# Performance work log

Hardware: AMD Instinct MI355X
Metric: run time of the kernel (lower is better)

Reference implementation:

```python
import jax, jax.numpy as jnp
import numpy as np

N_NODES = 100000
N_EDGES = 1600000
DIM = 128
N_LAYERS = 3


def setup_inputs() -> dict:
    key = jax.random.key(0)
    ks = jax.random.split(key, 8)
    h0 = jax.random.normal(ks[0], (N_NODES, 117), dtype=jnp.float32)
    src = jax.random.randint(ks[1], (N_EDGES,), 0, N_NODES, dtype=jnp.int32)
    dst = jax.random.randint(ks[2], (N_EDGES,), 0, N_NODES, dtype=jnp.int32)
    s_in = 1.0 / np.sqrt(117.0)
    s_h = 1.0 / np.sqrt(float(DIM))
    W_in = jax.random.uniform(ks[3], (117, DIM), jnp.float32, -s_in, s_in)
    b_in = jax.random.uniform(ks[4], (DIM,), jnp.float32, -s_in, s_in)
    W_self = jax.random.uniform(ks[5], (N_LAYERS, DIM, DIM), jnp.float32, -s_h, s_h)
    W_neigh = jax.random.uniform(ks[6], (N_LAYERS, DIM, DIM), jnp.float32, -s_h, s_h)
    b_sage = jax.random.uniform(ks[7], (N_LAYERS, DIM), jnp.float32, -s_h, s_h)
    return {"h0": h0, "src": src, "dst": dst, "W_in": W_in, "b_in": b_in,
            "W_self": W_self, "W_neigh": W_neigh, "b_sage": b_sage}


def _sage_mean(x, src, dst, Wse, Wne, b):
    # GraphSAGE with mean aggregator: h = x @ W_self + mean_neigh(x) @ W_neigh + b
    neigh_sum = jax.ops.segment_sum(x[src], dst, num_segments=N_NODES)  # [N, D]
    deg = jax.ops.segment_sum(jnp.ones((src.shape[0],), x.dtype), dst,
                              num_segments=N_NODES)  # [N]
    neigh_mean = neigh_sum / jnp.maximum(deg, 1.0)[:, None]
    return x @ Wse + neigh_mean @ Wne + b


def reference(h0, src, dst, W_in, b_in, W_self, W_neigh, b_sage):
    # f_in: Linear(117,128) + Tanh, per node
    h = jnp.tanh(h0 @ W_in + b_in)  # [N, 128]
    # config = [128,'relu'] x 3 -> SAGEConv then relu, three times
    for l in range(N_LAYERS):
        h = _sage_mean(h, src, dst, W_self[l], W_neigh[l], b_sage[l])
        h = jax.nn.relu(h)
    return h
```

## Files before the change

### kernel.cpp

```cpp
#include <hip/hip_runtime.h>
#include <hip/hip_bf16.h>
#include <cstdint>
#include <cstddef>

#define NN 100000
#define NE 1600000
#define DIM 128
#define KIN 117
#define NLAYERS 3
#define NB 98
#define NMAT 7

typedef __attribute__((ext_vector_type(8))) short s16x8;
typedef __attribute__((ext_vector_type(8))) __bf16 bf16x8;
typedef __attribute__((ext_vector_type(4))) float f32x4;

__device__ __forceinline__ unsigned short f2bf(float f) {
  unsigned int u = __float_as_uint(f);
  unsigned int r = (u + 0x7fffu + ((u >> 16) & 1u)) >> 16;
  return (unsigned short)r;
}
__device__ __forceinline__ float bf2f(unsigned short b) {
  return __uint_as_float(((unsigned int)b) << 16);
}


__global__ void k_hist(const int* __restrict__ dst, int* __restrict__ cnt) {
  int i = blockIdx.x * blockDim.x + threadIdx.x;
  if (i < NE) atomicAdd(&cnt[dst[i]], 1);
}

__global__ void k_scanA(const int* __restrict__ cnt, int* __restrict__ part,
                        int* __restrict__ bsum) {
  __shared__ int sh[1024];
  int tid = threadIdx.x;
  int i = blockIdx.x * 1024 + tid;
  int v = (i < NN) ? cnt[i] : 0;
  sh[tid] = v;
  __syncthreads();
  for (int off = 1; off < 1024; off <<= 1) {
    int t = (tid >= off) ? sh[tid - off] : 0;
    __syncthreads();
    sh[tid] += t;
    __syncthreads();
  }
  if (i < NN) part[i] = sh[tid] - v;
  if (tid == 1023) bsum[blockIdx.x] = sh[1023];
}

__global__ void k_scanB(const int* __restrict__ bsum, int* __restrict__ boff,
                        int* __restrict__ rptr) {
  if (threadIdx.x == 0 && blockIdx.x == 0) {
    int run = 0;
    for (int b = 0; b < NB; ++b) { boff[b] = run; run += bsum[b]; }
    rptr[NN] = run;
  }
}

__global__ void k_scanC(const int* __restrict__ part, const int* __restrict__ boff,
                        int* __restrict__ rptr, int* __restrict__ cursor) {
  int i = blockIdx.x * 1024 + threadIdx.x;
  if (i < NN) {
    int v = part[i] + boff[i >> 10];
    rptr[i] = v;
    cursor[i] = v;
  }
}

__global__ void k_scatter(const int* __restrict__ src, const int* __restrict__ dst,
                          int* __restrict__ cursor, int* __restrict__ ssrc) {
  int i = blockIdx.x * blockDim.x + threadIdx.x;
  if (i < NE) {
    int p = atomicAdd(&cursor[dst[i]], 1);
    ssrc[p] = src[i];
  }
}


__global__ __launch_bounds__(256) void k_agg(const float* __restrict__ x,
                                             const int* __restrict__ rptr,
                                             const int* __restrict__ ssrc,
                                             float* __restrict__ mean) {
  int gid = blockIdx.x * blockDim.x + threadIdx.x;
  int node = __builtin_amdgcn_readfirstlane(gid >> 6);
  int lane = threadIdx.x & 63;
  if (node >= NN) return;
  int beg = __builtin_amdgcn_readfirstlane(rptr[node]);
  int end = __builtin_amdgcn_readfirstlane(rptr[node + 1]);
  int c0 = lane * 2;
  float ax = 0.f, ay = 0.f;
  int e = beg;
  for (; e + 3 < end; e += 4) {
    int s0 = __builtin_amdgcn_readfirstlane(ssrc[e]);
    int s1 = __builtin_amdgcn_readfirstlane(ssrc[e + 1]);
    int s2 = __builtin_amdgcn_readfirstlane(ssrc[e + 2]);
    int s3 = __builtin_amdgcn_readfirstlane(ssrc[e + 3]);
    float2 v0 = *reinterpret_cast<const float2*>(x + (size_t)s0 * DIM + c0);
    float2 v1 = *reinterpret_cast<const float2*>(x + (size_t)s1 * DIM + c0);
    float2 v2 = *reinterpret_cast<const float2*>(x + (size_t)s2 * DIM + c0);
    float2 v3 = *reinterpret_cast<const float2*>(x + (size_t)s3 * DIM + c0);
    ax += (v0.x + v1.x) + (v2.x + v3.x);
    ay += (v0.y + v1.y) + (v2.y + v3.y);
  }
  for (; e < end; ++e) {
    int s0 = __builtin_amdgcn_readfirstlane(ssrc[e]);
    float2 v0 = *reinterpret_cast<const float2*>(x + (size_t)s0 * DIM + c0);
    ax += v0.x;
    ay += v0.y;
  }
  int deg = end - beg;
  float inv = 1.0f / (float)(deg > 0 ? deg : 1);
  *reinterpret_cast<float2*>(mean + (size_t)node * DIM + c0) =
      make_float2(ax * inv, ay * inv);
}


__global__ void k_wprep(const float* __restrict__ W_in,
                        const float* __restrict__ W_self,
                        const float* __restrict__ W_neigh,
                        unsigned short* __restrict__ Wfrag) {
  int bid = blockIdx.x;
  int mat = bid >> 7;
  int k = bid & 127;
  int col = threadIdx.x;
  float v = 0.f;
  if (mat == 0) {
    if (k < KIN) v = W_in[(size_t)k * DIM + col];
  } else if (mat <= 3) {
    v = W_self[(size_t)(mat - 1) * DIM * DIM + (size_t)k * DIM + col];
  } else {
    v = W_neigh[(size_t)(mat - 4) * DIM * DIM + (size_t)k * DIM + col];
  }
  unsigned short hb = f2bf(v);
  unsigned short lb = f2bf(v - bf2f(hb));
  int kt = k >> 5, k8 = (k >> 3) & 3, j = k & 7;
  size_t base = ((size_t)(mat * 4 + kt) * 2) * 4096 + ((size_t)k8 * 128 + col) * 8 + j;
  Wfrag[base] = hb;
  Wfrag[base + 4096] = lb;
}


template <int ACT, bool TWO>
__global__ __launch_bounds__(256) void k_gemm_mfma(
    const float* __restrict__ A, int lda, int Kvalid,
    const unsigned short* __restrict__ Wf0,
    const float* __restrict__ A2,
    const unsigned short* __restrict__ Wf1,
    const float* __restrict__ bias,
    float* __restrict__ out, int M) {
  __shared__ s16x8 Ah[512], Al[512], Bh[512], Bl[512];
  const int tid = threadIdx.x;
  const int lane = tid & 63;
  const int w = tid >> 6;
  const int wr = (w >> 1) * 64, wc = (w & 1) * 64;
  const int l15 = lane & 15, l4 = lane >> 4;
  const int m0 = blockIdx.x * 128;

  f32x4 acc[4][4];
#pragma unroll
  for (int r = 0; r < 4; ++r)
#pragma unroll
    for (int c = 0; c < 4; ++c) acc[r][c] = (f32x4){0.f, 0.f, 0.f, 0.f};

  const int srow = tid >> 1;
  const int shalf = tid & 1;

  for (int pass = 0; pass < (TWO ? 2 : 1); ++pass) {
    const float* Ap = pass ? A2 : A;
    const unsigned short* Wp = pass ? Wf1 : Wf0;
    const int ld = pass ? DIM : lda;
    const int Kv = pass ? DIM : Kvalid;
    for (int kt = 0; kt < 4; ++kt) {
      __syncthreads();
      {
        int kbase = kt * 32 + shalf * 16;
        float xv[16];
        const int row = m0 + srow;
        if (row < M && (ld & 3) == 0 && kbase + 16 <= Kv) {
          const float* sp = Ap + (size_t)row * ld + kbase;
#pragma unroll
          for (int q = 0; q < 4; ++q) {
            float4 v = *reinterpret_cast<const float4*>(sp + q * 4);
            xv[q * 4 + 0] = v.x; xv[q * 4 + 1] = v.y;
            xv[q * 4 + 2] = v.z; xv[q * 4 + 3] = v.w;
          }
        } else {
#pragma unroll
          for (int i = 0; i < 16; ++i) {
            int k = kbase + i;
            xv[i] = (row < M && k < Kv) ? Ap[(size_t)row * ld + k] : 0.f;
          }
        }
#pragma unroll
        for (int q = 0; q < 2; ++q) {
          s16x8 hv, lv;
#pragma unroll
          for (int j = 0; j < 8; ++j) {
            float xf = xv[q * 8 + j];
            unsigned short hb = f2bf(xf);
            unsigned short lb = f2bf(xf - bf2f(hb));
            hv[j] = (short)hb;
            lv[j] = (short)lb;
          }
          int slot = (2 * shalf + q) * 128 + srow;
          Ah[slot] = hv;
          Al[slot] = lv;
        }
      }
      {
        const s16x8* gW = reinterpret_cast<const s16x8*>(Wp + (size_t)kt * 8192);
#pragma unroll
        for (int r = 0; r < 2; ++r) {
          int s = r * 256 + tid;
          Bh[s] = gW[s];
          Bl[s] = gW[512 + s];
        }
      }
      __syncthreads();
      s16x8 ah[4], al_[4], bh[4], bl[4];
#pragma unroll
      for (int r = 0; r < 4; ++r) {
        int off = l4 * 128 + wr + r * 16 + l15;
        ah[r] = Ah[off];
        al_[r] = Al[off];
      }
#pragma unroll
      for (int c = 0; c < 4; ++c) {
        int off = l4 * 128 + wc + c * 16 + l15;
        bh[c] = Bh[off];
        bl[c] = Bl[off];
      }
#pragma unroll
      for (int r = 0; r < 4; ++r)
#pragma unroll
        for (int c = 0; c < 4; ++c) {
          acc[r][c] = __builtin_amdgcn_mfma_f32_16x16x32_bf16(
              __builtin_bit_cast(bf16x8, ah[r]), __builtin_bit_cast(bf16x8, bh[c]),
              acc[r][c], 0, 0, 0);
          acc[r][c] = __builtin_amdgcn_mfma_f32_16x16x32_bf16(
              __builtin_bit_cast(bf16x8, ah[r]), __builtin_bit_cast(bf16x8, bl[c]),
              acc[r][c], 0, 0, 0);
          acc[r][c] = __builtin_amdgcn_mfma_f32_16x16x32_bf16(
              __builtin_bit_cast(bf16x8, al_[r]), __builtin_bit_cast(bf16x8, bh[c]),
              acc[r][c], 0, 0, 0);
        }
    }
  }

#pragma unroll
  for (int c = 0; c < 4; ++c) {
    int col = wc + c * 16 + l15;
    float bv = bias[col];
#pragma unroll
    for (int r = 0; r < 4; ++r) {
#pragma unroll
      for (int i = 0; i < 4; ++i) {
        int row = m0 + wr + r * 16 + l4 * 4 + i;
        if (row < M) {
          float v = acc[r][c][i] + bv;
          if (ACT == 0) v = tanhf(v);
          else v = fmaxf(v, 0.f);
          out[(size_t)row * DIM + col] = v;
        }
      }
    }
  }
}


extern "C" void kernel_launch(void* const* d_in, const int* in_sizes, int n_in,
                              void* d_out, int out_size, void* d_ws, size_t ws_size,
                              hipStream_t stream) {
  const float* h0 = (const float*)d_in[0];
  const int* srcp = (const int*)d_in[1];
  const int* dstp = (const int*)d_in[2];
  const float* W_in = (const float*)d_in[3];
  const float* b_in = (const float*)d_in[4];
  const float* W_self = (const float*)d_in[5];
  const float* W_neigh = (const float*)d_in[6];
  const float* b_sage = (const float*)d_in[7];
  float* outf = (float*)d_out;

  char* p = (char*)d_ws;
  auto alloc = [&](size_t bytes) {
    char* r = p;
    p += (bytes + 255) & ~(size_t)255;
    return r;
  };
  float* mean = (float*)alloc((size_t)NN * DIM * 4);
  float* hA = (float*)alloc((size_t)NN * DIM * 4);
  int* cnt = (int*)alloc((size_t)NN * 4);
  int* part = (int*)alloc((size_t)NN * 4);
  int* rptr = (int*)alloc((size_t)(NN + 1) * 4);
  int* cursor = (int*)alloc((size_t)NN * 4);
  int* ssrcS = (int*)alloc((size_t)NE * 4);
  int* bsum = (int*)alloc((size_t)NB * 4);
  int* boff = (int*)alloc((size_t)NB * 4);
  unsigned short* Wfrag = (unsigned short*)alloc((size_t)NMAT * 4 * 2 * 4096 * 2);

  k_wprep<<<NMAT * 128, 128, 0, stream>>>(W_in, W_self, W_neigh, Wfrag);

  hipMemsetAsync(cnt, 0, (size_t)NN * 4, stream);
  k_hist<<<(NE + 255) / 256, 256, 0, stream>>>(dstp, cnt);
  k_scanA<<<NB, 1024, 0, stream>>>(cnt, part, bsum);
  k_scanB<<<1, 64, 0, stream>>>(bsum, boff, rptr);
  k_scanC<<<NB, 1024, 0, stream>>>(part, boff, rptr, cursor);
  k_scatter<<<(NE + 255) / 256, 256, 0, stream>>>(srcp, dstp, cursor, ssrcS);

  const int GB = (NN + 127) / 128;
  auto wmat = [&](int mat) { return Wfrag + (size_t)mat * 32768; };

  k_gemm_mfma<0, false><<<GB, 256, 0, stream>>>(h0, KIN, KIN, wmat(0), nullptr,
                                                nullptr, b_in, hA, NN);

  for (int l = 0; l < NLAYERS; ++l) {
    const float* x = (l == 1) ? outf : hA;
    float* o = (l == 1) ? hA : outf;
    const float* bs = b_sage + (size_t)l * DIM;
    k_agg<<<(NN * 64 + 255) / 256, 256, 0, stream>>>(x, rptr, ssrcS, mean);
    k_gemm_mfma<1, true><<<GB, 256, 0, stream>>>(x, DIM, DIM, wmat(1 + l), mean,
                                                 wmat(4 + l), bs, o, NN);
  }
}
```

Measured before the change: 845.2 us.

## Replace global atomic CSR scatter with two-pass bucketed partition

The per-edge global-atomic scatter into CSR order is replaced with a two-pass radix-style partition. The first pass sorts each 8192-edge chunk by 128-node bucket in shared memory, reserves space with one global atomic per bucket, and writes packed src/local-dst words contiguously. The second pass places edges within each bucket using shared-memory atomics. This cuts random global atomics and scattered writes, at the cost of an extra pass, a reused scratch buffer, and a per-edge binary search.

```diff
diff --git a/kernel.cpp b/kernel.cpp
--- a/kernel.cpp
+++ b/kernel.cpp
@@ -10,6 +10,9 @@
 #define NLAYERS 3
 #define NB 98
 #define NMAT 7
+#define NBUCK 782
+#define CH 8192
+#define P1B 196
 
 typedef __attribute__((ext_vector_type(8))) short s16x8;
 typedef __attribute__((ext_vector_type(8))) __bf16 bf16x8;
@@ -58,21 +61,100 @@
 }
 
 __global__ void k_scanC(const int* __restrict__ part, const int* __restrict__ boff,
-                        int* __restrict__ rptr, int* __restrict__ cursor) {
+                        int* __restrict__ rptr) {
   int i = blockIdx.x * 1024 + threadIdx.x;
-  if (i < NN) {
-    int v = part[i] + boff[i >> 10];
-    rptr[i] = v;
-    cursor[i] = v;
-  }
-}
-
-__global__ void k_scatter(const int* __restrict__ src, const int* __restrict__ dst,
-                          int* __restrict__ cursor, int* __restrict__ ssrc) {
-  int i = blockIdx.x * blockDim.x + threadIdx.x;
-  if (i < NE) {
-    int p = atomicAdd(&cursor[dst[i]], 1);
-    ssrc[p] = src[i];
+  if (i < NN) rptr[i] = part[i] + boff[i >> 10];
+}
+
+__global__ void k_initg(const int* __restrict__ rptr, int* __restrict__ gcur) {
+  int t = blockIdx.x * blockDim.x + threadIdx.x;
+  if (t < NBUCK) gcur[t] = rptr[t << 7];
+}
+
+__global__ __launch_bounds__(256) void k_part1(const int* __restrict__ src,
+                                               const int* __restrict__ dst,
+                                               int* __restrict__ gcur,
+                                               int* __restrict__ epart) {
+  __shared__ int hist[NBUCK];
+  __shared__ int lofs[NBUCK + 1];
+  __shared__ int cur[NBUCK];
+  __shared__ int base[NBUCK];
+  __shared__ int sorted[CH];
+  __shared__ int psum[256];
+  const int tid = threadIdx.x;
+  const int e0 = blockIdx.x * CH;
+  const int n = (NE - e0 < CH) ? (NE - e0) : CH;
+
+  for (int b = tid; b < NBUCK; b += 256) { hist[b] = 0; cur[b] = 0; }
+  __syncthreads();
+  for (int j = tid; j < n; j += 256)
+    atomicAdd(&hist[dst[e0 + j] >> 7], 1);
+  __syncthreads();
+  {
+    int b0 = tid * 4;
+    int loc[4];
+    int s = 0;
+    for (int q = 0; q < 4; ++q) {
+      int b = b0 + q;
+      loc[q] = s;
+      if (b < NBUCK) s += hist[b];
+    }
+    psum[tid] = s;
+    __syncthreads();
+    for (int off = 1; off < 256; off <<= 1) {
+      int t = (tid >= off) ? psum[tid - off] : 0;
+      __syncthreads();
+      psum[tid] += t;
+      __syncthreads();
+    }
+    int excl = (tid == 0) ? 0 : psum[tid - 1];
+    for (int q = 0; q < 4; ++q) {
+      int b = b0 + q;
+      if (b < NBUCK) lofs[b] = excl + loc[q];
+    }
+    if (tid == 0) lofs[NBUCK] = n;
+  }
+  __syncthreads();
+  for (int j = tid; j < n; j += 256) {
+    int d = dst[e0 + j];
+    int b = d >> 7;
+    int pos = atomicAdd(&cur[b], 1);
+    sorted[lofs[b] + pos] = (src[e0 + j] & 0x1FFFF) | ((d & 127) << 17);
+  }
+  for (int b = tid; b < NBUCK; b += 256) {
+    int h = hist[b];
+    if (h) base[b] = atomicAdd(&gcur[b], h);
+  }
+  __syncthreads();
+  for (int j = tid; j < n; j += 256) {
+    int lo = 0, hi = NBUCK;
+    while (hi - lo > 1) {
+      int mid = (lo + hi) >> 1;
+      if (lofs[mid] <= j) lo = mid; else hi = mid;
+    }
+    epart[base[lo] + (j - lofs[lo])] = sorted[j];
+  }
+}
+
+__global__ __launch_bounds__(256) void k_part2(const int* __restrict__ epart,
+                                               const int* __restrict__ rptr,
+                                               int* __restrict__ ssrc) {
+  __shared__ int curs[128];
+  const int b = blockIdx.x;
+  const int tid = threadIdx.x;
+  const int nb0 = b << 7;
+  if (tid < 128) {
+    int idx = nb0 + tid;
+    curs[tid] = (idx < NN) ? rptr[idx] : NE;
+  }
+  const int lo = rptr[nb0];
+  const int hi_idx = (nb0 + 128 < NN) ? (nb0 + 128) : NN;
+  const int hi = rptr[hi_idx];
+  __syncthreads();
+  for (int j = lo + tid; j < hi; j += 256) {
+    int w = epart[j];
+    int p = atomicAdd(&curs[(w >> 17) & 127], 1);
+    ssrc[p] = w & 0x1FFFF;
   }
 }
 
@@ -292,11 +374,12 @@
   int* cnt = (int*)alloc((size_t)NN * 4);
   int* part = (int*)alloc((size_t)NN * 4);
   int* rptr = (int*)alloc((size_t)(NN + 1) * 4);
-  int* cursor = (int*)alloc((size_t)NN * 4);
+  int* gcur = (int*)alloc((size_t)NBUCK * 4);
   int* ssrcS = (int*)alloc((size_t)NE * 4);
   int* bsum = (int*)alloc((size_t)NB * 4);
   int* boff = (int*)alloc((size_t)NB * 4);
   unsigned short* Wfrag = (unsigned short*)alloc((size_t)NMAT * 4 * 2 * 4096 * 2);
+  int* epart = (int*)mean;
 
   k_wprep<<<NMAT * 128, 128, 0, stream>>>(W_in, W_self, W_neigh, Wfrag);
 
@@ -304,8 +387,10 @@
   k_hist<<<(NE + 255) / 256, 256, 0, stream>>>(dstp, cnt);
   k_scanA<<<NB, 1024, 0, stream>>>(cnt, part, bsum);
   k_scanB<<<1, 64, 0, stream>>>(bsum, boff, rptr);
-  k_scanC<<<NB, 1024, 0, stream>>>(part, boff, rptr, cursor);
-  k_scatter<<<(NE + 255) / 256, 256, 0, stream>>>(srcp, dstp, cursor, ssrcS);
+  k_scanC<<<NB, 1024, 0, stream>>>(part, boff, rptr);
+  k_initg<<<(NBUCK + 255) / 256, 256, 0, stream>>>(rptr, gcur);
+  k_part1<<<P1B, 256, 0, stream>>>(srcp, dstp, gcur, epart);
+  k_part2<<<NBUCK, 256, 0, stream>>>(epart, rptr, ssrcS);
 
   const int GB = (NN + 127) / 128;
   auto wmat = [&](int mat) { return Wfrag + (size_t)mat * 32768; };
```

After: 821.1 us. -2.9%, faster.
